# Kernel optimization log

Hardware: AMD Instinct MI355X
Metric: run time of the kernel (lower is better)

## Reference

```python
import jax, jax.numpy as jnp
import numpy as np

EPS = 1e-10
TWO_PI = 2.0 * np.pi


def _nll(y_target, o_pred):
    # getCoef: split last dim of o_pred into 5 bivariate-Gaussian params
    mux = o_pred[..., 0]
    muy = o_pred[..., 1]
    sx = jnp.exp(o_pred[..., 2])
    sy = jnp.exp(o_pred[..., 3])
    corr = jnp.tanh(o_pred[..., 4])

    norm_x = (y_target[..., 1] - mux) / sx
    norm_y = (y_target[..., 2] - muy) / sy
    z = norm_x ** 2 + norm_y ** 2 - 2.0 * corr * norm_x * norm_y
    onemrho = 1.0 - corr ** 2
    top = jnp.exp(-z / (2.0 * onemrho))
    bottom = TWO_PI * (sx * sy * jnp.sqrt(onemrho))
    pdf = top / bottom  # (B, T, P)

    # sum over all (b, t, p) of -log(clamp(pdf, eps)), divided by ped_num
    total = jnp.sum(-jnp.log(jnp.clip(pdf, EPS)))
    return total / pdf.shape[2]


def setup_inputs() -> dict:
    key = jax.random.key(0)
    k1, k2 = jax.random.split(key)
    B, T, P = 64, 128, 512
    y_target = jax.random.normal(k1, (B, T, P, 3), dtype=jnp.float32)
    o_pred = jax.random.normal(k2, (B, T, P, 5), dtype=jnp.float32)
    return {"y_target": y_target, "o_pred": o_pred}


def reference(y_target, o_pred):
    return _nll(y_target, o_pred)
```

## Files before the change

### kernel.cpp

```cpp
#include <hip/hip_runtime.h>
#include <hip/hip_bf16.h>


#define THREADS 256
#define PPT 4
#define TILE (THREADS * PPT)

__device__ __forceinline__ float point_nll(float mux, float muy, float lsx,
                                           float lsy, float w, float y1, float y2) {
    const float LOG_2PI = 1.8378770664093453f;
    const float CLIP    = 23.025850929940457f;
    float isx  = __expf(-lsx);
    float isy  = __expf(-lsy);
    float nx   = (y1 - mux) * isx;
    float ny   = (y2 - muy) * isy;
    float corr = tanhf(w);
    float omr  = fmaf(-corr, corr, 1.0f);
    float z    = fmaf(nx, nx, ny * ny) - 2.0f * corr * nx * ny;
    float nll  = z / (2.0f * omr) + LOG_2PI + lsx + lsy + 0.5f * __logf(omr);
    return fminf(nll, CLIP);
}

__global__ __launch_bounds__(THREADS) void nll_partial_kernel(
    const float* __restrict__ y, const float* __restrict__ o,
    float* __restrict__ partial, int N) {
    __shared__ float4 lds_o[5 * THREADS];
    __shared__ float4 lds_y[3 * THREADS];

    const int tid = threadIdx.x;
    const long long base_pt = (long long)blockIdx.x * TILE;
    float acc = 0.0f;

    if (base_pt + TILE <= (long long)N) {
        const float4* o4 = (const float4*)o + base_pt * 5 / 4;
        const float4* y4 = (const float4*)y + base_pt * 3 / 4;
#pragma unroll
        for (int k = 0; k < 5; ++k) lds_o[k * THREADS + tid] = o4[k * THREADS + tid];
#pragma unroll
        for (int k = 0; k < 3; ++k) lds_y[k * THREADS + tid] = y4[k * THREADS + tid];
        __syncthreads();

        const float* fo = (const float*)lds_o + tid * (PPT * 5);
        const float* fy = (const float*)lds_y + tid * (PPT * 3);
#pragma unroll
        for (int j = 0; j < PPT; ++j) {
            acc += point_nll(fo[5 * j + 0], fo[5 * j + 1], fo[5 * j + 2],
                             fo[5 * j + 3], fo[5 * j + 4],
                             fy[3 * j + 1], fy[3 * j + 2]);
        }
    } else {
        long long i0 = base_pt + (long long)tid * PPT;
        for (int j = 0; j < PPT; ++j) {
            long long i = i0 + j;
            if (i < (long long)N)
                acc += point_nll(o[i * 5 + 0], o[i * 5 + 1], o[i * 5 + 2],
                                 o[i * 5 + 3], o[i * 5 + 4],
                                 y[i * 3 + 1], y[i * 3 + 2]);
        }
    }

#pragma unroll
    for (int off = 32; off > 0; off >>= 1) acc += __shfl_down(acc, off, 64);
    __shared__ float ws[THREADS / 64];
    if ((tid & 63) == 0) ws[tid >> 6] = acc;
    __syncthreads();
    if (tid == 0) {
        float s = 0.0f;
#pragma unroll
        for (int i = 0; i < THREADS / 64; ++i) s += ws[i];
        partial[blockIdx.x] = s;
    }
}

__global__ __launch_bounds__(THREADS) void nll_final_kernel(
    const float* __restrict__ partial, int nparts, float* __restrict__ out,
    float inv_p) {
    float acc = 0.0f;
    for (int i = threadIdx.x; i < nparts; i += THREADS) acc += partial[i];
#pragma unroll
    for (int off = 32; off > 0; off >>= 1) acc += __shfl_down(acc, off, 64);
    __shared__ float ws[THREADS / 64];
    if ((threadIdx.x & 63) == 0) ws[threadIdx.x >> 6] = acc;
    __syncthreads();
    if (threadIdx.x == 0) {
        float s = 0.0f;
#pragma unroll
        for (int i = 0; i < THREADS / 64; ++i) s += ws[i];
        out[0] = s * inv_p;
    }
}

extern "C" void kernel_launch(void* const* d_in, const int* in_sizes, int n_in,
                              void* d_out, int out_size, void* d_ws, size_t ws_size,
                              hipStream_t stream) {
    const float* y = (const float*)d_in[0];
    const float* o = (const float*)d_in[1];
    int N = in_sizes[1] / 5;
    int blocks = (N + TILE - 1) / TILE;

    float* partial = (float*)d_ws;
    nll_partial_kernel<<<blocks, THREADS, 0, stream>>>(y, o, partial, N);
    nll_final_kernel<<<1, THREADS, 0, stream>>>(partial, blocks, (float*)d_out,
                                                1.0f / 512.0f);
}
```

Measured before the change: 161.6 us.

## Replace LDS-staged tile loads with grid-stride direct loads and cheaper tanh

Drops the shared-memory staging of float4 tiles and replaces it with a grid-stride loop capped at 2048 blocks, where each thread loads its point's five o values and two y values straight from global memory, four points ahead. tanh is computed from exp plus a hardware reciprocal, and the division is replaced by a reciprocal multiply. The direct per-thread loads use strides of 20 and 12 bytes, so they are not coalesced like the old float4 loads, and this may cost more bandwidth than removing the LDS round trip and the barrier saves. The tanh formula can overflow to inf for large w, though it still gives the right limit of 1.

```diff
diff --git a/kernel.cpp b/kernel.cpp
--- a/kernel.cpp
+++ b/kernel.cpp
@@ -3,8 +3,7 @@
 
 
 #define THREADS 256
-#define PPT 4
-#define TILE (THREADS * PPT)
+#define UNROLL 4
 
 __device__ __forceinline__ float point_nll(float mux, float muy, float lsx,
                                            float lsy, float w, float y1, float y2) {
@@ -14,48 +13,44 @@
     float isy  = __expf(-lsy);
     float nx   = (y1 - mux) * isx;
     float ny   = (y2 - muy) * isy;
-    float corr = tanhf(w);
+    float e2w  = __expf(2.0f * w);
+    float corr = fmaf(-2.0f, __builtin_amdgcn_rcpf(e2w + 1.0f), 1.0f);
     float omr  = fmaf(-corr, corr, 1.0f);
     float z    = fmaf(nx, nx, ny * ny) - 2.0f * corr * nx * ny;
-    float nll  = z / (2.0f * omr) + LOG_2PI + lsx + lsy + 0.5f * __logf(omr);
+    float nll  = fmaf(z, 0.5f * __builtin_amdgcn_rcpf(omr),
+                      fmaf(0.5f, __logf(omr), lsx + lsy + LOG_2PI));
     return fminf(nll, CLIP);
 }
 
-__global__ __launch_bounds__(THREADS) void nll_partial_kernel(
+__global__ __launch_bounds__(THREADS, 4) void nll_partial_kernel(
     const float* __restrict__ y, const float* __restrict__ o,
     float* __restrict__ partial, int N) {
-    __shared__ float4 lds_o[5 * THREADS];
-    __shared__ float4 lds_y[3 * THREADS];
-
     const int tid = threadIdx.x;
-    const long long base_pt = (long long)blockIdx.x * TILE;
+    const long long T = (long long)gridDim.x * THREADS;
     float acc = 0.0f;
 
-    if (base_pt + TILE <= (long long)N) {
-        const float4* o4 = (const float4*)o + base_pt * 5 / 4;
-        const float4* y4 = (const float4*)y + base_pt * 3 / 4;
+    for (long long p0 = (long long)blockIdx.x * THREADS + tid; p0 < (long long)N;
+         p0 += T * UNROLL) {
+        float ov[UNROLL][5], yv1[UNROLL], yv2[UNROLL];
+        bool ok[UNROLL];
 #pragma unroll
-        for (int k = 0; k < 5; ++k) lds_o[k * THREADS + tid] = o4[k * THREADS + tid];
+        for (int j = 0; j < UNROLL; ++j) {
+            long long p = p0 + (long long)j * T;
+            ok[j] = (p < (long long)N);
+            if (ok[j]) {
+                const float* op = o + p * 5;
+                const float* yp = y + p * 3;
 #pragma unroll
-        for (int k = 0; k < 3; ++k) lds_y[k * THREADS + tid] = y4[k * THREADS + tid];
-        __syncthreads();
-
-        const float* fo = (const float*)lds_o + tid * (PPT * 5);
-        const float* fy = (const float*)lds_y + tid * (PPT * 3);
+                for (int c = 0; c < 5; ++c) ov[j][c] = op[c];
+                yv1[j] = yp[1];
+                yv2[j] = yp[2];
+            }
+        }
 #pragma unroll
-        for (int j = 0; j < PPT; ++j) {
-            acc += point_nll(fo[5 * j + 0], fo[5 * j + 1], fo[5 * j + 2],
-                             fo[5 * j + 3], fo[5 * j + 4],
-                             fy[3 * j + 1], fy[3 * j + 2]);
-        }
-    } else {
-        long long i0 = base_pt + (long long)tid * PPT;
-        for (int j = 0; j < PPT; ++j) {
-            long long i = i0 + j;
-            if (i < (long long)N)
-                acc += point_nll(o[i * 5 + 0], o[i * 5 + 1], o[i * 5 + 2],
-                                 o[i * 5 + 3], o[i * 5 + 4],
-                                 y[i * 3 + 1], y[i * 3 + 2]);
+        for (int j = 0; j < UNROLL; ++j) {
+            if (ok[j])
+                acc += point_nll(ov[j][0], ov[j][1], ov[j][2], ov[j][3], ov[j][4],
+                                 yv1[j], yv2[j]);
         }
     }
 
@@ -96,7 +91,9 @@
     const float* y = (const float*)d_in[0];
     const float* o = (const float*)d_in[1];
     int N = in_sizes[1] / 5;
-    int blocks = (N + TILE - 1) / TILE;
+    int max_blocks = (N + THREADS * UNROLL - 1) / (THREADS * UNROLL);
+    int blocks = max_blocks < 2048 ? max_blocks : 2048;
+    if (blocks < 1) blocks = 1;
 
     float* partial = (float*)d_ws;
     nll_partial_kernel<<<blocks, THREADS, 0, stream>>>(y, o, partial, N);
```

Measured after the change: 162.3 us. No clear change (+0.4%).
